# Kernel optimization log

Measured on AMD Instinct MI355X. Metric: run time of the kernel, lower is better.

The kernel has to match this reference:

```python
import jax, jax.numpy as jnp
import numpy as np

E, K, H, I, GS, T, C = 64, 4, 2048, 1536, 128, 1024, 128

# FP4 E2M1 lookup table: sign bit in nibble MSB, magnitudes {0,.5,1,1.5,2,3,4,6}
LUT = jnp.array([0.0, 0.5, 1.0, 1.5, 2.0, 3.0, 4.0, 6.0,
                 -0.0, -0.5, -1.0, -1.5, -2.0, -3.0, -4.0, -6.0], dtype=jnp.float32)


def _dequant(packed, scales):
    """packed: [O, I//8] int32 (8 FP4 nibbles/word), scales: [I//GS, O] -> W [O, I] fp32."""
    O, IW = packed.shape
    shifts = (jnp.arange(8, dtype=jnp.int32) * 4)
    nib = (packed[:, :, None] >> shifts) & 0xF          # [O, IW, 8]
    vals = LUT[nib].reshape(O, IW * 8)                   # [O, I]
    g = jnp.arange(IW * 8) // GS                         # group index per input col
    return vals * scales.T[:, g]                         # [O, I]


def _mlp(x2d, gp, gs, up, us, dp, ds):
    """SwiGLU expert: down( silu(x Wg^T) * (x Wu^T) )."""
    Wg = _dequant(gp, gs)
    Wu = _dequant(up, us)
    Wd = _dequant(dp, ds)
    h = jax.nn.silu(x2d @ Wg.T) * (x2d @ Wu.T)           # [N, I]
    return h @ Wd.T                                      # [N, H]


def setup_inputs() -> dict:
    key = jax.random.key(0)
    ks = jax.random.split(key, 16)
    ri = lambda k, sh: jax.random.randint(k, sh, 0, 2**31 - 1, dtype=jnp.int32)
    sc = lambda k, sh: jax.random.uniform(k, sh, dtype=jnp.float32) * 0.02 + 0.001
    return {
        "x": jax.random.normal(ks[0], (T, H), dtype=jnp.float32),
        "gate_w": jax.random.normal(ks[1], (E, H), dtype=jnp.float32) * 0.02,
        "gate_scales": sc(ks[2], (E, H // GS, I)),
        "up_scales": sc(ks[3], (E, H // GS, I)),
        "down_scales": sc(ks[4], (E, I // GS, H)),
        "sh_gate_scales": sc(ks[5], (H // GS, I)),
        "sh_up_scales": sc(ks[6], (H // GS, I)),
        "sh_down_scales": sc(ks[7], (I // GS, H)),
        "gate_packed": ri(ks[8], (E, I, H // 8)),
        "up_packed": ri(ks[9], (E, I, H // 8)),
        "down_packed": ri(ks[10], (E, H, I // 8)),
        "sh_gate_packed": ri(ks[11], (I, H // 8)),
        "sh_up_packed": ri(ks[12], (I, H // 8)),
        "sh_down_packed": ri(ks[13], (H, I // 8)),
    }


def reference(x, gate_w, gate_scales, up_scales, down_scales,
              sh_gate_scales, sh_up_scales, sh_down_scales,
              gate_packed, up_packed, down_packed,
              sh_gate_packed, sh_up_packed, sh_down_packed):
    # --- top-k routing ---
    probs = jax.nn.softmax(x @ gate_w.T, axis=-1)        # [T, E]
    tw, ti = jax.lax.top_k(probs, K)                     # [T, K]
    tw = tw / tw.sum(-1, keepdims=True)
    # --- dispatch with fixed capacity C per expert ---
    A = T * K
    ef = ti.reshape(-1)                                  # [A] expert id per assignment
    tok = jnp.arange(A) // K                             # source token per assignment
    counts = jax.ops.segment_sum(jnp.ones(A, jnp.int32), ef, num_segments=E)
    starts = jnp.cumsum(counts) - counts                 # [E]
    sidx = jnp.argsort(ef)
    pos_sorted = jnp.arange(A, dtype=jnp.int32) - starts[ef[sidx]]
    pos = jnp.zeros(A, jnp.int32).at[sidx].set(pos_sorted)  # rank within expert
    slot = ef * C + pos
    valid = pos < C
    buf = jnp.zeros((E * C + 1, H), x.dtype).at[jnp.where(valid, slot, E * C)].set(x[tok])
    buf = buf[:E * C].reshape(E, C, H)
    # --- per-expert fused dequant + SwiGLU (scan over experts) ---
    def body(_, xs):
        b, gp, gs, up, us, dp, ds = xs
        return None, _mlp(b, gp, gs, up, us, dp, ds)
    _, eout = jax.lax.scan(body, None,
                           (buf, gate_packed, gate_scales, up_packed, up_scales,
                            down_packed, down_scales))
    # --- combine ---
    rows = eout.reshape(E * C, H)
    gath = rows[jnp.where(valid, slot, 0)] * valid[:, None].astype(x.dtype)
    y = (gath.reshape(T, K, H) * tw[..., None]).sum(axis=1)
    # --- shared expert ---
    y = y + _mlp(x, sh_gate_packed, sh_gate_scales, sh_up_packed, sh_up_scales,
                 sh_down_packed, sh_down_scales)
    return y
```

## Files before the change

kernel.cpp:

```cpp
#include <hip/hip_runtime.h>
#include <stdint.h>

#define E_ 64
#define KTOP 4
#define H_ 2048
#define I_ 1536
#define GS_ 128
#define T_ 1024
#define CAP 128

typedef __attribute__((ext_vector_type(8))) short short8;
typedef __attribute__((ext_vector_type(4))) float f32x4;

__device__ __forceinline__ uint32_t bf16rne(float f) {
  uint32_t u = __float_as_uint(f);
  return (u + 0x7FFFu + ((u >> 16) & 1u)) >> 16;
}
__device__ __forceinline__ float bf16f(uint32_t b) {
  return __uint_as_float(b << 16);
}

__global__ void cast_x_kernel(const float* __restrict__ x, uint16_t* __restrict__ xb, int n4) {
  int i = blockIdx.x * blockDim.x + threadIdx.x;
  if (i >= n4) return;
  float4 v = ((const float4*)x)[i];
  uint32_t lo = bf16rne(v.x) | (bf16rne(v.y) << 16);
  uint32_t hi = bf16rne(v.z) | (bf16rne(v.w) << 16);
  uint2 r; r.x = lo; r.y = hi;
  ((uint2*)xb)[i] = r;
}

__global__ void transpose_gw_kernel(const float* __restrict__ gw, float* __restrict__ gwT) {
  int o = blockIdx.x * 256 + threadIdx.x;
  int k = o >> 6, e = o & 63;
  gwT[o] = gw[(long)e * H_ + k];
}

__global__ __launch_bounds__(256) void routing_kernel(
    const float* __restrict__ x, const float* __restrict__ gwT,
    float* __restrict__ tw, int* __restrict__ ti) {
  int t = blockIdx.x;
  int tid = threadIdx.x;
  __shared__ float xs[H_];
  __shared__ float lgp[4][E_];
  const float4* xp = (const float4*)(x + (long)t * H_);
  ((float4*)xs)[tid] = xp[tid];
  ((float4*)xs)[tid + 256] = xp[tid + 256];
  __syncthreads();
  int e = tid & 63, w4 = tid >> 6;
  const float* gp = gwT + (long)w4 * 512 * E_ + e;
  const float* xw = xs + w4 * 512;
  float a0 = 0.f, a1 = 0.f, a2 = 0.f, a3 = 0.f;
#pragma unroll 4
  for (int k = 0; k < 512; k += 4) {
    a0 += xw[k]     * gp[(long)(k)     * E_];
    a1 += xw[k + 1] * gp[(long)(k + 1) * E_];
    a2 += xw[k + 2] * gp[(long)(k + 2) * E_];
    a3 += xw[k + 3] * gp[(long)(k + 3) * E_];
  }
  lgp[w4][e] = (a0 + a1) + (a2 + a3);
  __syncthreads();
  if (tid < 64) {
    int lane = tid;
    float v = lgp[0][lane] + lgp[1][lane] + lgp[2][lane] + lgp[3][lane];
    float vals[KTOP]; int ids[KTOP];
#pragma unroll
    for (int k = 0; k < KTOP; k++) {
      float bv = v; int bi = lane;
      for (int off = 32; off; off >>= 1) {
        float ov = __shfl_xor(bv, off);
        int oi = __shfl_xor(bi, off);
        if (ov > bv || (ov == bv && oi < bi)) { bv = ov; bi = oi; }
      }
      vals[k] = bv; ids[k] = bi;
      if (lane == bi) v = -3.4e38f;
    }
    if (lane == 0) {
      float m = vals[0];
      float p[KTOP]; float s = 0.f;
#pragma unroll
      for (int k = 0; k < KTOP; k++) { p[k] = expf(vals[k] - m); s += p[k]; }
      float inv = 1.f / s;
#pragma unroll
      for (int k = 0; k < KTOP; k++) {
        tw[t * KTOP + k] = p[k] * inv;
        ti[t * KTOP + k] = ids[k];
      }
    }
  }
}

__global__ void assign_kernel(const int* __restrict__ ti, int* __restrict__ counts,
                              int* __restrict__ tlist, int* __restrict__ slot_of) {
  int e = blockIdx.x;
  int lane = threadIdx.x;
  int cnt = 0;
  for (int base = 0; base < T_ * KTOP; base += 64) {
    int a = base + lane;
    int ef = ti[a];
    unsigned long long m = __ballot(ef == e);
    if (ef == e) {
      int rank = cnt + __popcll(m & ((1ull << lane) - 1ull));
      if (rank < CAP) {
        tlist[e * CAP + rank] = a >> 2;
        slot_of[a] = e * CAP + rank;
      } else {
        slot_of[a] = -1;
      }
    }
    cnt += __popcll(m);
  }
  if (lane == 0) counts[e] = min(cnt, CAP);
}

template <int OUTF32>
__global__ __launch_bounds__(256, 2) void gemm_fp4_kernel(
    const uint16_t* __restrict__ A, int ldA,
    const int* __restrict__ rowids, const int* __restrict__ counts,
    const int* __restrict__ packed, long p_stride,
    const float* __restrict__ scales, long s_stride,
    void* __restrict__ outp, int K, int N, int row_stride_e) {
  __shared__ uint16_t As[128 * 128];
  __shared__ uint16_t Bs[16 * 128 * 8];
  __shared__ int rowid_s[128];

  int e = blockIdx.z, mb = blockIdx.y, bn = blockIdx.x;
  int tid = threadIdx.x;
  int wave = tid >> 6, lane = tid & 63;

  int row_base = e * row_stride_e + mb * 128;
  int valid = 128;
  if (counts) {
    valid = counts[e] - mb * 128;
    if (valid <= 0) return;
    if (valid > 128) valid = 128;
  }
  if (tid < 128) {
    int rr = tid < valid ? tid : valid - 1;
    rowid_s[tid] = rowids ? rowids[row_base + rr] : row_base + rr;
  }

  const int* packed_e = packed + (long)e * p_stride;
  const float* scales_e = scales + (long)e * s_stride;

  int j = tid >> 1;
  int wseg = tid & 1;
  int n_col = bn * 128 + j;
  const int* prow = packed_e + (long)n_col * (K >> 3) + wseg * 8;

  f32x4 acc[4][4];
#pragma unroll
  for (int a0 = 0; a0 < 4; a0++)
#pragma unroll
    for (int b0 = 0; b0 < 4; b0++) {
      f32x4 z = {0.f, 0.f, 0.f, 0.f};
      acc[a0][b0] = z;
    }

  int wm = wave >> 1, wn = wave & 1;
  int q = lane >> 4;
  int r16 = lane & 15;

  __syncthreads();

  for (int kt = 0; kt < K; kt += 128) {
#pragma unroll
    for (int ii = 0; ii < 8; ii++) {
      int inst = wave * 8 + ii;
      int r = inst * 4 + (lane >> 4);
      int c = lane & 15;
      int g = c ^ (r & 15);
      const uint16_t* src = A + (long)rowid_s[r] * ldA + kt + (g << 3);
      __builtin_amdgcn_global_load_lds(
          (const __attribute__((address_space(1))) unsigned int*)src,
          (__attribute__((address_space(3))) unsigned int*)(As + inst * 512),
          16, 0, 0);
    }
    {
      float s = scales_e[(long)(kt >> 7) * N + n_col];
      uint32_t b1 = bf16rne(s), b15 = bf16rne(1.5f * s);
      uint32_t t0 = 0, t1 = b1 - 0x80, t2 = b1, t3 = b15;
      uint32_t t4 = b1 + 0x80, t5 = b15 + 0x80, t6 = b1 + 0x100, t7 = b15 + 0x100;
      uint32_t tll = (t0 & 0xFF) | ((t1 & 0xFF) << 8) | ((t2 & 0xFF) << 16) | ((t3 & 0xFF) << 24);
      uint32_t tlh = (t4 & 0xFF) | ((t5 & 0xFF) << 8) | ((t6 & 0xFF) << 16) | ((t7 & 0xFF) << 24);
      uint32_t thl = (t0 >> 8) | ((t1 >> 8) << 8) | ((t2 >> 8) << 16) | ((t3 >> 8) << 24);
      uint32_t thh = (t4 >> 8) | ((t5 >> 8) << 8) | ((t6 >> 8) << 16) | ((t7 >> 8) << 24);

      const int4* pv = (const int4*)(prow + (kt >> 3));
      int4 wA = pv[0];
      int4 wB = pv[1];
      uint32_t wsv[8] = {(uint32_t)wA.x, (uint32_t)wA.y, (uint32_t)wA.z, (uint32_t)wA.w,
                         (uint32_t)wB.x, (uint32_t)wB.y, (uint32_t)wB.z, (uint32_t)wB.w};
      uint16_t* bdst = Bs + ((long)(wseg * 8) * 128 + j) * 8;
#pragma unroll
      for (int i = 0; i < 8; i++) {
        uint32_t w = wsv[i];
        uint32_t ev = w & 0x07070707u;
        uint32_t od = (w >> 4) & 0x07070707u;
        uint32_t se = (w << 4) & 0x80808080u;
        uint32_t so = w & 0x80808080u;
        uint32_t he = __builtin_amdgcn_perm(thh, thl, ev) | se;
        uint32_t ho = __builtin_amdgcn_perm(thh, thl, od) | so;
        uint32_t le = __builtin_amdgcn_perm(tlh, tll, ev);
        uint32_t lo = __builtin_amdgcn_perm(tlh, tll, od);
        uint32_t v02 = __builtin_amdgcn_perm(he, le, 0x05010400u);
        uint32_t v46 = __builtin_amdgcn_perm(he, le, 0x07030602u);
        uint32_t v13 = __builtin_amdgcn_perm(ho, lo, 0x05010400u);
        uint32_t v57 = __builtin_amdgcn_perm(ho, lo, 0x07030602u);
        uint4 qv;
        qv.x = __builtin_amdgcn_perm(v13, v02, 0x05040100u);
        qv.y = __builtin_amdgcn_perm(v13, v02, 0x07060302u);
        qv.z = __builtin_amdgcn_perm(v57, v46, 0x05040100u);
        qv.w = __builtin_amdgcn_perm(v57, v46, 0x07060302u);
        *(uint4*)(bdst + (long)i * 1024) = qv;
      }
    }
    __syncthreads();

#pragma unroll
    for (int kk = 0; kk < 128; kk += 32) {
      int kc = (kk >> 3) + q;
      short8 af[4], bfr[4];
#pragma unroll
      for (int fm = 0; fm < 4; fm++) {
        int m = wm * 64 + fm * 16 + r16;
        af[fm] = *(const short8*)(As + (long)m * 128 + ((kc ^ r16) << 3));
      }
#pragma unroll
      for (int fn = 0; fn < 4; fn++) {
        int n = wn * 64 + fn * 16 + r16;
        bfr[fn] = *(const short8*)(Bs + ((long)kc * 128 + n) * 8);
      }
#pragma unroll
      for (int fm = 0; fm < 4; fm++)
#pragma unroll
        for (int fn = 0; fn < 4; fn++)
          acc[fm][fn] = __builtin_amdgcn_mfma_f32_16x16x32_bf16(af[fm], bfr[fn], acc[fm][fn], 0, 0, 0);
    }
    __syncthreads();
  }

  int outr0 = wm * 64 + (q << 2);
  int outc0 = bn * 128 + wn * 64 + r16;
#pragma unroll
  for (int fm = 0; fm < 4; fm++)
#pragma unroll
    for (int fn = 0; fn < 4; fn++) {
#pragma unroll
      for (int r = 0; r < 4; r++) {
        int rloc = outr0 + fm * 16 + r;
        if (rloc >= valid) continue;
        long row = row_base + rloc;
        long col = outc0 + fn * 16;
        float vv = acc[fm][fn][r];
        if (OUTF32) ((float*)outp)[row * N + col] = vv;
        else ((uint16_t*)outp)[row * N + col] = (uint16_t)bf16rne(vv);
      }
    }
}

__global__ void silu_mul_kernel(const uint16_t* __restrict__ g, const uint16_t* __restrict__ u,
                                uint16_t* __restrict__ h, int n8) {
  int i = blockIdx.x * blockDim.x + threadIdx.x;
  if (i >= n8) return;
  uint4 gv = ((const uint4*)g)[i];
  uint4 uv = ((const uint4*)u)[i];
  uint32_t gw[4] = {gv.x, gv.y, gv.z, gv.w};
  uint32_t uw[4] = {uv.x, uv.y, uv.z, uv.w};
  uint32_t rw[4];
#pragma unroll
  for (int w = 0; w < 4; w++) {
    float g0 = bf16f(gw[w] & 0xFFFFu), g1 = bf16f(gw[w] >> 16);
    float u0 = bf16f(uw[w] & 0xFFFFu), u1 = bf16f(uw[w] >> 16);
    float r0 = g0 / (1.f + __expf(-g0)) * u0;
    float r1 = g1 / (1.f + __expf(-g1)) * u1;
    rw[w] = bf16rne(r0) | (bf16rne(r1) << 16);
  }
  uint4 res; res.x = rw[0]; res.y = rw[1]; res.z = rw[2]; res.w = rw[3];
  ((uint4*)h)[i] = res;
}

__global__ __launch_bounds__(256) void combine_kernel(
    float* __restrict__ y, const uint16_t* __restrict__ eout,
    const int* __restrict__ slot_of, const float* __restrict__ tw) {
  int t = blockIdx.x;
  int c = threadIdx.x * 8;
  float* yp = y + (long)t * H_ + c;
  float4 y0 = ((float4*)yp)[0];
  float4 y1 = ((float4*)yp)[1];
  float a[8] = {y0.x, y0.y, y0.z, y0.w, y1.x, y1.y, y1.z, y1.w};
#pragma unroll
  for (int k = 0; k < KTOP; k++) {
    int s = slot_of[t * KTOP + k];
    float w = tw[t * KTOP + k];
    if (s < 0) continue;
    uint4 v = *(const uint4*)(eout + (long)s * H_ + c);
    uint32_t vw[4] = {v.x, v.y, v.z, v.w};
#pragma unroll
    for (int jj = 0; jj < 4; jj++) {
      a[2 * jj]     += w * bf16f(vw[jj] & 0xFFFFu);
      a[2 * jj + 1] += w * bf16f(vw[jj] >> 16);
    }
  }
  float4 o0 = {a[0], a[1], a[2], a[3]};
  float4 o1 = {a[4], a[5], a[6], a[7]};
  ((float4*)yp)[0] = o0;
  ((float4*)yp)[1] = o1;
}

extern "C" void kernel_launch(void* const* d_in, const int* in_sizes, int n_in,
                              void* d_out, int out_size, void* d_ws, size_t ws_size,
                              hipStream_t stream) {
  const float* x              = (const float*)d_in[0];
  const float* gate_w         = (const float*)d_in[1];
  const float* gate_scales    = (const float*)d_in[2];
  const float* up_scales      = (const float*)d_in[3];
  const float* down_scales    = (const float*)d_in[4];
  const float* sh_gate_scales = (const float*)d_in[5];
  const float* sh_up_scales   = (const float*)d_in[6];
  const float* sh_down_scales = (const float*)d_in[7];
  const int* gate_packed      = (const int*)d_in[8];
  const int* up_packed        = (const int*)d_in[9];
  const int* down_packed      = (const int*)d_in[10];
  const int* sh_gate_packed   = (const int*)d_in[11];
  const int* sh_up_packed     = (const int*)d_in[12];
  const int* sh_down_packed   = (const int*)d_in[13];
  float* y = (float*)d_out;

  char* ws = (char*)d_ws;
  uint16_t* xb     = (uint16_t*)(ws);
  float*    tw     = (float*)(ws + 4194304);
  int*      ti     = (int*)(ws + 4210688);
  int*      counts = (int*)(ws + 4227072);
  int*      tlist  = (int*)(ws + 4227328);
  int*      slot_of= (int*)(ws + 4260096);
  uint16_t* gbuf   = (uint16_t*)(ws + 4276480);
  float*    gwT    = (float*)(ws + 4276480);
  uint16_t* ubuf   = (uint16_t*)(ws + 29442304);
  uint16_t* eout   = (uint16_t*)(ws + 29442304);
  uint16_t* gsbuf  = (uint16_t*)(ws + 62996736);
  uint16_t* usbuf  = (uint16_t*)(ws + 66142464);

  cast_x_kernel<<<2048, 256, 0, stream>>>(x, xb, T_ * H_ / 4);
  transpose_gw_kernel<<<512, 256, 0, stream>>>(gate_w, gwT);
  routing_kernel<<<T_, 256, 0, stream>>>(x, gwT, tw, ti);
  assign_kernel<<<E_, 64, 0, stream>>>(ti, counts, tlist, slot_of);

  gemm_fp4_kernel<0><<<dim3(12, 1, 64), 256, 0, stream>>>(
      xb, H_, tlist, counts, gate_packed, (long)I_ * (H_ / 8), gate_scales, (long)(H_ / GS_) * I_,
      gbuf, H_, I_, CAP);
  gemm_fp4_kernel<0><<<dim3(12, 1, 64), 256, 0, stream>>>(
      xb, H_, tlist, counts, up_packed, (long)I_ * (H_ / 8), up_scales, (long)(H_ / GS_) * I_,
      ubuf, H_, I_, CAP);
  silu_mul_kernel<<<(E_ * CAP * I_ / 8 + 255) / 256, 256, 0, stream>>>(
      gbuf, ubuf, gbuf, E_ * CAP * I_ / 8);
  gemm_fp4_kernel<0><<<dim3(16, 1, 64), 256, 0, stream>>>(
      gbuf, I_, nullptr, counts, down_packed, (long)H_ * (I_ / 8), down_scales, (long)(I_ / GS_) * H_,
      eout, I_, H_, CAP);

  gemm_fp4_kernel<0><<<dim3(12, 8, 1), 256, 0, stream>>>(
      xb, H_, nullptr, nullptr, sh_gate_packed, 0, sh_gate_scales, 0,
      gsbuf, H_, I_, 0);
  gemm_fp4_kernel<0><<<dim3(12, 8, 1), 256, 0, stream>>>(
      xb, H_, nullptr, nullptr, sh_up_packed, 0, sh_up_scales, 0,
      usbuf, H_, I_, 0);
  silu_mul_kernel<<<(T_ * I_ / 8 + 255) / 256, 256, 0, stream>>>(
      gsbuf, usbuf, gsbuf, T_ * I_ / 8);
  gemm_fp4_kernel<1><<<dim3(16, 8, 1), 256, 0, stream>>>(
      gsbuf, I_, nullptr, nullptr, sh_down_packed, 0, sh_down_scales, 0,
      y, I_, H_, 0);

  combine_kernel<<<T_, 256, 0, stream>>>(y, eout, slot_of, tw);
}
```

Before: 647.6 us.

## Double-buffer GEMM K-loop and merge routed and shared expert launches

The FP4 GEMM now steps K in 64-wide tiles with double-buffered A tiles in LDS. The next tile's A rows and packed weights are prefetched while the current tile is dequantized and run through MFMA, and explicit waitcnt/barrier plus setprio control the ordering. Shared-expert blocks are folded into the same grid as the routed experts, so each gate/up/down stage is one launch instead of two. Launch bounds rise to 3 blocks per CU thanks to the smaller LDS footprint. The cost is more barriers per K step and hand-tuned vmcnt values that must match the number of outstanding loads.

New measurement: 546.1 us. -15.7%, faster.

```diff
diff --git a/kernel.cpp b/kernel.cpp
--- a/kernel.cpp
+++ b/kernel.cpp
@@ -113,40 +113,64 @@
   if (lane == 0) counts[e] = min(cnt, CAP);
 }
 
-template <int OUTF32>
-__global__ __launch_bounds__(256, 2) void gemm_fp4_kernel(
-    const uint16_t* __restrict__ A, int ldA,
-    const int* __restrict__ rowids, const int* __restrict__ counts,
-    const int* __restrict__ packed, long p_stride,
-    const float* __restrict__ scales, long s_stride,
-    void* __restrict__ outp, int K, int N, int row_stride_e) {
-  __shared__ uint16_t As[128 * 128];
-  __shared__ uint16_t Bs[16 * 128 * 8];
-  __shared__ int rowid_s[128];
-
-  int e = blockIdx.z, mb = blockIdx.y, bn = blockIdx.x;
+__global__ __launch_bounds__(256, 3) void gemm_fp4_kernel(
+    const uint16_t* __restrict__ A1, const uint16_t* __restrict__ A2, int ldA,
+    const int* __restrict__ rowids, const int* __restrict__ counts, int nE,
+    const int* __restrict__ packed1, long p_stride,
+    const float* __restrict__ scales1, long s_stride,
+    const int* __restrict__ packed2, const float* __restrict__ scales2,
+    void* __restrict__ out1, int of1, void* __restrict__ out2, int of2,
+    int K, int N) {
+  __shared__ uint16_t As[2][128 * 64];
+  __shared__ uint16_t Bs[8 * 128 * 8];
+
+  int yb = blockIdx.y, bn = blockIdx.x;
   int tid = threadIdx.x;
   int wave = tid >> 6, lane = tid & 63;
 
-  int row_base = e * row_stride_e + mb * 128;
-  int valid = 128;
-  if (counts) {
-    valid = counts[e] - mb * 128;
+  const uint16_t* A;
+  const int* packed_e;
+  const float* scales_e;
+  char* outp;
+  int of32, row_base, valid;
+  const int* rid = nullptr;
+  if (yb < nE) {
+    int e = yb;
+    valid = counts[e];
     if (valid <= 0) return;
     if (valid > 128) valid = 128;
-  }
-  if (tid < 128) {
-    int rr = tid < valid ? tid : valid - 1;
-    rowid_s[tid] = rowids ? rowids[row_base + rr] : row_base + rr;
-  }
-
-  const int* packed_e = packed + (long)e * p_stride;
-  const float* scales_e = scales + (long)e * s_stride;
-
-  int j = tid >> 1;
-  int wseg = tid & 1;
+    if (rowids) rid = rowids + e * CAP;
+    row_base = e * CAP;
+    A = A1;
+    packed_e = packed1 + (long)e * p_stride;
+    scales_e = scales1 + (long)e * s_stride;
+    outp = (char*)out1; of32 = of1;
+  } else {
+    valid = 128;
+    row_base = (yb - nE) * 128;
+    A = A2;
+    packed_e = packed2;
+    scales_e = scales2;
+    outp = (char*)out2; of32 = of2;
+  }
+
+  const uint16_t* asrc[4];
+  int adst[4];
+#pragma unroll
+  for (int ii = 0; ii < 4; ii++) {
+    int inst = wave * 4 + ii;
+    int r = inst * 8 + (lane >> 3);
+    int rr = r < valid ? r : valid - 1;
+    long arow = rid ? (long)rid[rr] : (long)(row_base + rr);
+    int g = (lane & 7) ^ (r & 7);
+    asrc[ii] = A + arow * (long)ldA + (g << 3);
+    adst[ii] = inst * 512;
+  }
+
+  int j = tid >> 1, wseg = tid & 1;
   int n_col = bn * 128 + j;
-  const int* prow = packed_e + (long)n_col * (K >> 3) + wseg * 8;
+  const int* prow = packed_e + (long)n_col * (K >> 3) + wseg * 4;
+  uint16_t* bdst = Bs + ((long)(wseg * 4) * 128 + j) * 8;
 
   f32x4 acc[4][4];
 #pragma unroll
@@ -158,26 +182,38 @@
     }
 
   int wm = wave >> 1, wn = wave & 1;
-  int q = lane >> 4;
-  int r16 = lane & 15;
-
-  __syncthreads();
-
-  for (int kt = 0; kt < K; kt += 128) {
-#pragma unroll
-    for (int ii = 0; ii < 8; ii++) {
-      int inst = wave * 8 + ii;
-      int r = inst * 4 + (lane >> 4);
-      int c = lane & 15;
-      int g = c ^ (r & 15);
-      const uint16_t* src = A + (long)rowid_s[r] * ldA + kt + (g << 3);
-      __builtin_amdgcn_global_load_lds(
-          (const __attribute__((address_space(1))) unsigned int*)src,
-          (__attribute__((address_space(3))) unsigned int*)(As + inst * 512),
-          16, 0, 0);
+  int q = lane >> 4, r16 = lane & 15;
+
+  int nk = K >> 6;
+
+  uint4 bpk_c = *(const uint4*)prow;
+  float scl_c = scales_e[n_col];
+#pragma unroll
+  for (int ii = 0; ii < 4; ii++)
+    __builtin_amdgcn_global_load_lds(
+        (const __attribute__((address_space(1))) unsigned int*)asrc[ii],
+        (__attribute__((address_space(3))) unsigned int*)(&As[0][0] + adst[ii]),
+        16, 0, 0);
+  uint4 bpk_n = bpk_c;
+  float scl_n = scl_c;
+
+  for (int it = 0; it < nk; ++it) {
+    int b = it & 1;
+    int kt2 = (it + 1) << 6;
+    int pf = (it + 1 < nk);
+    if (pf) {
+      bpk_n = *(const uint4*)(prow + (kt2 >> 3));
+      scl_n = scales_e[(long)(kt2 >> 7) * N + n_col];
+      uint16_t* ab = &As[b ^ 1][0];
+#pragma unroll
+      for (int ii = 0; ii < 4; ii++)
+        __builtin_amdgcn_global_load_lds(
+            (const __attribute__((address_space(1))) unsigned int*)(asrc[ii] + kt2),
+            (__attribute__((address_space(3))) unsigned int*)(ab + adst[ii]),
+            16, 0, 0);
     }
     {
-      float s = scales_e[(long)(kt >> 7) * N + n_col];
+      float s = scl_c;
       uint32_t b1 = bf16rne(s), b15 = bf16rne(1.5f * s);
       uint32_t t0 = 0, t1 = b1 - 0x80, t2 = b1, t3 = b15;
       uint32_t t4 = b1 + 0x80, t5 = b15 + 0x80, t6 = b1 + 0x100, t7 = b15 + 0x100;
@@ -185,20 +221,14 @@
       uint32_t tlh = (t4 & 0xFF) | ((t5 & 0xFF) << 8) | ((t6 & 0xFF) << 16) | ((t7 & 0xFF) << 24);
       uint32_t thl = (t0 >> 8) | ((t1 >> 8) << 8) | ((t2 >> 8) << 16) | ((t3 >> 8) << 24);
       uint32_t thh = (t4 >> 8) | ((t5 >> 8) << 8) | ((t6 >> 8) << 16) | ((t7 >> 8) << 24);
-
-      const int4* pv = (const int4*)(prow + (kt >> 3));
-      int4 wA = pv[0];
-      int4 wB = pv[1];
-      uint32_t wsv[8] = {(uint32_t)wA.x, (uint32_t)wA.y, (uint32_t)wA.z, (uint32_t)wA.w,
-                         (uint32_t)wB.x, (uint32_t)wB.y, (uint32_t)wB.z, (uint32_t)wB.w};
-      uint16_t* bdst = Bs + ((long)(wseg * 8) * 128 + j) * 8;
-#pragma unroll
-      for (int i = 0; i < 8; i++) {
-        uint32_t w = wsv[i];
-        uint32_t ev = w & 0x07070707u;
-        uint32_t od = (w >> 4) & 0x07070707u;
-        uint32_t se = (w << 4) & 0x80808080u;
-        uint32_t so = w & 0x80808080u;
+      uint32_t wsv[4] = {bpk_c.x, bpk_c.y, bpk_c.z, bpk_c.w};
+#pragma unroll
+      for (int w = 0; w < 4; w++) {
+        uint32_t wv = wsv[w];
+        uint32_t ev = wv & 0x07070707u;
+        uint32_t od = (wv >> 4) & 0x07070707u;
+        uint32_t se = (wv << 4) & 0x80808080u;
+        uint32_t so = wv & 0x80808080u;
         uint32_t he = __builtin_amdgcn_perm(thh, thl, ev) | se;
         uint32_t ho = __builtin_amdgcn_perm(thh, thl, od) | so;
         uint32_t le = __builtin_amdgcn_perm(tlh, tll, ev);
@@ -212,24 +242,30 @@
         qv.y = __builtin_amdgcn_perm(v13, v02, 0x07060302u);
         qv.z = __builtin_amdgcn_perm(v57, v46, 0x05040100u);
         qv.w = __builtin_amdgcn_perm(v57, v46, 0x07060302u);
-        *(uint4*)(bdst + (long)i * 1024) = qv;
-      }
-    }
-    __syncthreads();
-
-#pragma unroll
-    for (int kk = 0; kk < 128; kk += 32) {
-      int kc = (kk >> 3) + q;
+        *(uint4*)(bdst + (long)w * 1024) = qv;
+      }
+    }
+    if (pf) asm volatile("s_waitcnt vmcnt(6) lgkmcnt(0)" ::: "memory");
+    else    asm volatile("s_waitcnt vmcnt(0) lgkmcnt(0)" ::: "memory");
+    __builtin_amdgcn_sched_barrier(0);
+    __builtin_amdgcn_s_barrier();
+    __builtin_amdgcn_sched_barrier(0);
+
+    const uint16_t* asb = &As[b][0];
+    __builtin_amdgcn_s_setprio(1);
+#pragma unroll
+    for (int kk = 0; kk < 64; kk += 32) {
+      int kc4 = (kk >> 3) + q;
       short8 af[4], bfr[4];
 #pragma unroll
       for (int fm = 0; fm < 4; fm++) {
         int m = wm * 64 + fm * 16 + r16;
-        af[fm] = *(const short8*)(As + (long)m * 128 + ((kc ^ r16) << 3));
+        af[fm] = *(const short8*)(asb + (long)m * 64 + ((kc4 ^ (m & 7)) << 3));
       }
 #pragma unroll
       for (int fn = 0; fn < 4; fn++) {
         int n = wn * 64 + fn * 16 + r16;
-        bfr[fn] = *(const short8*)(Bs + ((long)kc * 128 + n) * 8);
+        bfr[fn] = *(const short8*)(Bs + ((long)kc4 * 128 + n) * 8);
       }
 #pragma unroll
       for (int fm = 0; fm < 4; fm++)
@@ -237,7 +273,12 @@
         for (int fn = 0; fn < 4; fn++)
           acc[fm][fn] = __builtin_amdgcn_mfma_f32_16x16x32_bf16(af[fm], bfr[fn], acc[fm][fn], 0, 0, 0);
     }
-    __syncthreads();
+    __builtin_amdgcn_s_setprio(0);
+    __builtin_amdgcn_sched_barrier(0);
+    __builtin_amdgcn_s_barrier();
+    __builtin_amdgcn_sched_barrier(0);
+    bpk_c = bpk_n;
+    scl_c = scl_n;
   }
 
   int outr0 = wm * 64 + (q << 2);
@@ -253,7 +294,7 @@
         long row = row_base + rloc;
         long col = outc0 + fn * 16;
         float vv = acc[fm][fn][r];
-        if (OUTF32) ((float*)outp)[row * N + col] = vv;
+        if (of32) ((float*)outp)[row * N + col] = vv;
         else ((uint16_t*)outp)[row * N + col] = (uint16_t)bf16rne(vv);
       }
     }
@@ -346,29 +387,27 @@
   routing_kernel<<<T_, 256, 0, stream>>>(x, gwT, tw, ti);
   assign_kernel<<<E_, 64, 0, stream>>>(ti, counts, tlist, slot_of);
 
-  gemm_fp4_kernel<0><<<dim3(12, 1, 64), 256, 0, stream>>>(
-      xb, H_, tlist, counts, gate_packed, (long)I_ * (H_ / 8), gate_scales, (long)(H_ / GS_) * I_,
-      gbuf, H_, I_, CAP);
-  gemm_fp4_kernel<0><<<dim3(12, 1, 64), 256, 0, stream>>>(
-      xb, H_, tlist, counts, up_packed, (long)I_ * (H_ / 8), up_scales, (long)(H_ / GS_) * I_,
-      ubuf, H_, I_, CAP);
+  gemm_fp4_kernel<<<dim3(12, 72, 1), 256, 0, stream>>>(
+      xb, xb, H_, tlist, counts, E_,
+      gate_packed, (long)I_ * (H_ / 8), gate_scales, (long)(H_ / GS_) * I_,
+      sh_gate_packed, sh_gate_scales,
+      gbuf, 0, gsbuf, 0, H_, I_);
+  gemm_fp4_kernel<<<dim3(12, 72, 1), 256, 0, stream>>>(
+      xb, xb, H_, tlist, counts, E_,
+      up_packed, (long)I_ * (H_ / 8), up_scales, (long)(H_ / GS_) * I_,
+      sh_up_packed, sh_up_scales,
+      ubuf, 0, usbuf, 0, H_, I_);
+
   silu_mul_kernel<<<(E_ * CAP * I_ / 8 + 255) / 256, 256, 0, stream>>>(
       gbuf, ubuf, gbuf, E_ * CAP * I_ / 8);
-  gemm_fp4_kernel<0><<<dim3(16, 1, 64), 256, 0, stream>>>(
-      gbuf, I_, nullptr, counts, down_packed, (long)H_ * (I_ / 8), down_scales, (long)(I_ / GS_) * H_,
-      eout, I_, H_, CAP);
-
-  gemm_fp4_kernel<0><<<dim3(12, 8, 1), 256, 0, stream>>>(
-      xb, H_, nullptr, nullptr, sh_gate_packed, 0, sh_gate_scales, 0,
-      gsbuf, H_, I_, 0);
-  gemm_fp4_kernel<0><<<dim3(12, 8, 1), 256, 0, stream>>>(
-      xb, H_, nullptr, nullptr, sh_up_packed, 0, sh_up_scales, 0,
-      usbuf, H_, I_, 0);
   silu_mul_kernel<<<(T_ * I_ / 8 + 255) / 256, 256, 0, stream>>>(
       gsbuf, usbuf, gsbuf, T_ * I_ / 8);
-  gemm_fp4_kernel<1><<<dim3(16, 8, 1), 256, 0, stream>>>(
-      gsbuf, I_, nullptr, nullptr, sh_down_packed, 0, sh_down_scales, 0,
-      y, I_, H_, 0);
+
+  gemm_fp4_kernel<<<dim3(16, 72, 1), 256, 0, stream>>>(
+      gbuf, gsbuf, I_, nullptr, counts, E_,
+      down_packed, (long)H_ * (I_ / 8), down_scales, (long)(I_ / GS_) * H_,
+      sh_down_packed, sh_down_scales,
+      eout, 0, y, 1, I_, H_);
 
   combine_kernel<<<T_, 256, 0, stream>>>(y, eout, slot_of, tw);
 }
```
